# Kernel tuning notes

Hardware: AMD Instinct MI355X
Metric: run time of the kernel (lower is better)

## Reference

```python
import jax, jax.numpy as jnp
import numpy as np

D = 64       # feature_dim
C = 64       # number of classes
NS = 1024    # support samples (16 shots per class)
NQ = 32768   # query samples
REG = 0.3    # reg_param
KAPPA0 = 1.0 / 600.0  # gamma_m from _num_images=600


def _l2norm(x):
    # torch F.normalize(p=2, dim=1) with eps=1e-12
    return x / jnp.maximum(jnp.linalg.norm(x, axis=1, keepdims=True), 1e-12)


def setup_inputs() -> dict:
    key = jax.random.key(0)
    k1, k2 = jax.random.split(key)
    return {
        "X_support": jax.random.normal(k1, (NS, D), dtype=jnp.float32),
        "y_support": jnp.arange(NS, dtype=jnp.int32) % C,  # every class populated
        "X_query": jax.random.normal(k2, (NQ, D), dtype=jnp.float32),
        "m": jnp.zeros((D,), dtype=jnp.float32),            # zeros * gamma_m
        "S": jnp.eye(D, dtype=jnp.float32),                  # eye * gamma_S
        "nu": jnp.float32(float(D)),
        "kappa": jnp.float32(KAPPA0),
    }


def reference(X_support, y_support, X_query, m, S, nu, kappa):
    # ---- fit ----
    Xs = _l2norm(X_support)                                   # [NS, D]
    onehot = jax.nn.one_hot(y_support, C, dtype=Xs.dtype)     # [NS, C]
    Nj = onehot.sum(axis=0)                                   # [C] per-class counts
    means = (onehot.T @ Xs) / Nj[:, None]                     # [C, D] class means
    N0 = Nj[0]                                                # original uses class-0 count
    # head_mu_eq is vector + scalar broadcast, exactly as the torch code
    head = kappa / (kappa + N0) * m + N0 / (kappa + N0)       # [D]
    mu = head[None, :] * means                                # [C, D] elementwise product
    L = S * jnp.tril(jnp.ones((D, D), dtype=Xs.dtype))        # triu(ones).t() mask
    middle = L @ L.T                                          # [D, D]
    Ssum = jnp.einsum('nj,nd,ne->jde', onehot, Xs, Xs)        # sum of outer products per class
    left = 1.0 / (nu + Nj + D + 2)                            # [C]
    mmT = kappa * jnp.outer(m, m)                             # [D, D]
    mu_outer = jnp.einsum('jd,je->jde', mu, mu)               # [C, D, D]
    right = middle[None] + Ssum + mmT[None] - (kappa + Nj)[:, None, None] * mu_outer
    sigma = left[:, None, None] * right                       # [C, D, D]
    A = (1.0 - REG) * jnp.linalg.inv(sigma) + REG * jnp.eye(D, dtype=Xs.dtype)

    # ---- predict: -(x - mu_j)^T A_j (x - mu_j), A_j symmetric ----
    Xq = _l2norm(X_query)                                     # [NQ, D]
    Amu = jnp.einsum('jde,je->jd', A, mu)                     # [C, D]
    cross = Xq @ Amu.T                                        # [NQ, C]
    muAmu = jnp.einsum('jd,jd->j', mu, Amu)                   # [C]
    XA = jnp.einsum('nd,jde->nje', Xq, A)                     # [NQ, C, D]
    quad = jnp.einsum('nje,ne->nj', XA, Xq)                   # [NQ, C]
    return -(quad - 2.0 * cross + muAmu[None, :])             # [NQ, C]
```

## Files before the change

### kernel.cpp

```cpp
#include <hip/hip_runtime.h>
#include <stdint.h>

#define NSUP 1024
#define NQRY 32768
#define DIM  64
#define NCLS 64

typedef float  f32x4  __attribute__((ext_vector_type(4)));
typedef short  s16x8  __attribute__((ext_vector_type(8)));
typedef __bf16 bf16x8 __attribute__((ext_vector_type(8)));

static __device__ __forceinline__ unsigned short f2bf(float f) {
  unsigned u = __float_as_uint(f);
  u += 0x7FFFu + ((u >> 16) & 1u);
  return (unsigned short)(u >> 16);
}

__global__ __launch_bounds__(256) void prep_and_mid(
    const float* __restrict__ Xq, const float* __restrict__ mg,
    const float* __restrict__ Sg, const float* __restrict__ kapg,
    unsigned short* __restrict__ Ybf, float* __restrict__ Mid2) {
  __shared__ float Sls[64 * 65];
  __shared__ float mls[64];
  int tid = threadIdx.x;

  if (blockIdx.x < 2048) {
    int lane = tid & 63;
    int wave = tid >> 6;
    int row  = blockIdx.x * 16 + wave * 4 + (lane >> 4);
    int cb   = (lane & 15) * 4;
    float4 v = *(const float4*)(Xq + (size_t)row * 64 + cb);
    float ss = v.x * v.x + v.y * v.y + v.z * v.z + v.w * v.w;
    ss += __shfl_xor(ss, 1);
    ss += __shfl_xor(ss, 2);
    ss += __shfl_xor(ss, 4);
    ss += __shfl_xor(ss, 8);
    float inv = 1.0f / fmaxf(sqrtf(ss), 1e-12f);
    unsigned short a = f2bf(v.x * inv), b = f2bf(v.y * inv);
    unsigned short c = f2bf(v.z * inv), d = f2bf(v.w * inv);
    uint2 o;
    o.x = (unsigned)a | ((unsigned)b << 16);
    o.y = (unsigned)c | ((unsigned)d << 16);
    *(uint2*)(Ybf + (size_t)row * 64 + cb) = o;
    return;
  }

  for (int i = tid; i < 4096; i += 256) Sls[(i >> 6) * 65 + (i & 63)] = Sg[i];
  if (tid < 64) mls[tid] = mg[tid];
  __syncthreads();
  float kap = kapg[0];
  int r_ = tid & 63, cblk = tid >> 6, c0 = cblk * 16;
#pragma unroll 1
  for (int i = 0; i < 16; ++i) {
    int cc = c0 + i;
    int kmax = min(r_, cc);
    float mid = 0.f;
    for (int k = 0; k <= kmax; ++k) mid += Sls[r_ * 65 + k] * Sls[cc * 65 + k];
    Mid2[r_ * 64 + cc] = mid + kap * mls[r_] * mls[cc];
  }
}

__global__ __launch_bounds__(256) void fit_classes(
    const float* __restrict__ Xs, const int* __restrict__ ys,
    const float* __restrict__ mg, const float* __restrict__ Mid2,
    const float* __restrict__ nug, const float* __restrict__ kapg,
    unsigned short* __restrict__ LtG, float* __restrict__ Bg) {
  __shared__ float xsch[16][68];
  __shared__ float muls[64];
  __shared__ float fcol[2][64];
  __shared__ float prow[2][64];
  __shared__ float Lls[64 * 65];
  __shared__ int   lst[64];
  __shared__ int   cnts[2];

  int tid = threadIdx.x;
  int j   = blockIdx.x;
  int rr = tid >> 2, cq = tid & 3, cc0 = cq * 16;

  if (tid < 64) {
    int lane = tid;
    int cnt = 0, n0 = 0;
    for (int b = 0; b < NSUP; b += 64) {
      int yv = ys[b + lane];
      unsigned long long mj = __ballot(yv == j);
      unsigned long long m0 = __ballot(yv == 0);
      if (lane == 0) {
        n0 += (int)__popcll(m0);
        while (mj && cnt < 64) { int bit = __builtin_ctzll(mj); lst[cnt++] = b + bit; mj &= mj - 1; }
      }
    }
    if (lane == 0) { cnts[0] = cnt; cnts[1] = n0; }
  }
  __syncthreads();
  int cnt = cnts[0], n0 = cnts[1];

  float acc[16];
  {
    const float* mrow = Mid2 + rr * 64 + cc0;
    float4 m0 = *(const float4*)(mrow + 0);
    float4 m1 = *(const float4*)(mrow + 4);
    float4 m2 = *(const float4*)(mrow + 8);
    float4 m3 = *(const float4*)(mrow + 12);
    acc[0]=m0.x; acc[1]=m0.y; acc[2]=m0.z; acc[3]=m0.w;
    acc[4]=m1.x; acc[5]=m1.y; acc[6]=m1.z; acc[7]=m1.w;
    acc[8]=m2.x; acc[9]=m2.y; acc[10]=m2.z; acc[11]=m2.w;
    acc[12]=m3.x; acc[13]=m3.y; acc[14]=m3.z; acc[15]=m3.w;
  }

  float sumx = 0.f;
  for (int s0 = 0; s0 < cnt; s0 += 16) {
    int nch = min(16, cnt - s0);
    int s = tid >> 4, f = tid & 15;
    if (s < nch) {
      int n = lst[s0 + s];
      float4 v = *(const float4*)(Xs + (size_t)n * 64 + f * 4);
      float ss = v.x * v.x + v.y * v.y + v.z * v.z + v.w * v.w;
      ss += __shfl_xor(ss, 1); ss += __shfl_xor(ss, 2);
      ss += __shfl_xor(ss, 4); ss += __shfl_xor(ss, 8);
      float inv = 1.0f / fmaxf(sqrtf(ss), 1e-12f);
      xsch[s][f * 4 + 0] = v.x * inv;
      xsch[s][f * 4 + 1] = v.y * inv;
      xsch[s][f * 4 + 2] = v.z * inv;
      xsch[s][f * 4 + 3] = v.w * inv;
    }
    __syncthreads();
    for (int s2 = 0; s2 < nch; ++s2) {
      float ar = xsch[s2][rr];
      sumx += ar;
#pragma unroll
      for (int i = 0; i < 16; ++i) acc[i] += ar * xsch[s2][cc0 + i];
    }
    __syncthreads();
  }

  float kap = kapg[0], nuv = nug[0];
  float Njf = (float)cnt, N0f = (float)n0;
  float mean_r = sumx / Njf;
  float head_r = kap / (kap + N0f) * mg[rr] + N0f / (kap + N0f);
  float mu_r = head_r * mean_r;
  if (cq == 0) muls[rr] = mu_r;
  __syncthreads();

  float a[16];
  {
    float left = 1.0f / (nuv + Njf + (float)DIM + 2.0f);
    float kn = kap + Njf;
#pragma unroll
    for (int i = 0; i < 16; ++i)
      a[i] = left * (acc[i] - kn * mu_r * muls[cc0 + i]);
  }

  {
    float fsel = 0.f;
#pragma unroll
    for (int i = 0; i < 16; ++i) fsel = (cc0 + i == 0) ? a[i] : fsel;
    if (cq == 0) fcol[0][rr] = fsel;
    if (rr == 0) {
#pragma unroll
      for (int i = 0; i < 16; ++i) prow[0][cc0 + i] = a[i];
    }
  }
  __syncthreads();

  for (int p = 0; p < 64; ++p) {
    int pb = p & 1;
    float d  = 1.0f / fcol[pb][p];
    float fr = fcol[pb][rr];
#pragma unroll
    for (int i = 0; i < 16; ++i) {
      int c = cc0 + i;
      float q  = prow[pb][c] * d;
      float ar = a[i];
      float res;
      if (rr == p) res = (c == p) ? d : q;
      else         res = (c == p) ? (-fr * d) : fmaf(-fr, q, ar);
      a[i] = res;
    }
    if (p < 63) {
      float fsel = 0.f;
#pragma unroll
      for (int i = 0; i < 16; ++i) fsel = (cc0 + i == p + 1) ? a[i] : fsel;
      if (cq == ((p + 1) >> 4)) fcol[pb ^ 1][rr] = fsel;
      if (rr == p + 1) {
#pragma unroll
        for (int i = 0; i < 16; ++i) prow[pb ^ 1][cc0 + i] = a[i];
      }
    }
    __syncthreads();
  }

#pragma unroll
  for (int i = 0; i < 16; ++i)
    a[i] = 0.7f * a[i] + ((cc0 + i == rr) ? 0.3f : 0.f);
  {
    float fsel = 0.f;
#pragma unroll
    for (int i = 0; i < 16; ++i) fsel = (cc0 + i == 0) ? a[i] : fsel;
    if (cq == 0) fcol[0][rr] = fsel;
  }
  __syncthreads();

  for (int k = 0; k < 64; ++k) {
    int pb = k & 1;
    float akk = fcol[pb][k];
    float rs  = 1.0f / sqrtf(akk);
    float vr  = fcol[pb][rr] * rs;
#pragma unroll
    for (int i = 0; i < 16; ++i) {
      int c = cc0 + i;
      if (c == k)              a[i] = (rr >= k) ? vr : 0.f;
      else if (rr > k && c > k) a[i] -= vr * (fcol[pb][c] * rs);
    }
    if (k < 63) {
      float fsel = 0.f;
#pragma unroll
      for (int i = 0; i < 16; ++i) fsel = (cc0 + i == k + 1) ? a[i] : fsel;
      if (cq == ((k + 1) >> 4)) fcol[pb ^ 1][rr] = fsel;
    }
    __syncthreads();
  }

#pragma unroll
  for (int i = 0; i < 16; ++i) {
    int c = cc0 + i;
    Lls[rr * 65 + c] = (c <= rr) ? a[i] : 0.f;
  }
  __syncthreads();
  {
    unsigned short tmp[16];
#pragma unroll
    for (int i = 0; i < 16; ++i) tmp[i] = f2bf(Lls[(cc0 + i) * 65 + rr]);
    uint4 w0, w1;
    w0.x = (unsigned)tmp[0]  | ((unsigned)tmp[1]  << 16);
    w0.y = (unsigned)tmp[2]  | ((unsigned)tmp[3]  << 16);
    w0.z = (unsigned)tmp[4]  | ((unsigned)tmp[5]  << 16);
    w0.w = (unsigned)tmp[6]  | ((unsigned)tmp[7]  << 16);
    w1.x = (unsigned)tmp[8]  | ((unsigned)tmp[9]  << 16);
    w1.y = (unsigned)tmp[10] | ((unsigned)tmp[11] << 16);
    w1.z = (unsigned)tmp[12] | ((unsigned)tmp[13] << 16);
    w1.w = (unsigned)tmp[14] | ((unsigned)tmp[15] << 16);
    *(uint4*)(LtG + j * 4096 + rr * 64 + cc0)     = w0;
    *(uint4*)(LtG + j * 4096 + rr * 64 + cc0 + 8) = w1;
  }
  {
    float s = 0.f;
#pragma unroll
    for (int i = 0; i < 16; ++i) s += Lls[(cc0 + i) * 65 + rr] * muls[cc0 + i];
    s += __shfl_xor(s, 1);
    s += __shfl_xor(s, 2);
    if (cq == 0) Bg[j * 64 + rr] = s;
  }
}

__global__ __launch_bounds__(256) void predict_kernel(
    const unsigned short* __restrict__ Ybf, const unsigned short* __restrict__ Lt,
    const float* __restrict__ Bg, float* __restrict__ out) {
  int tid   = threadIdx.x;
  int lane  = tid & 63;
  int wave  = tid >> 6;
  int qt    = blockIdx.x >> 2;
  int cg    = blockIdx.x & 3;
  int cbase = cg * 16;
  int qbase = qt * 256 + wave * 64;
  int c = lane & 15, h = lane >> 4;

  s16x8 bfr[4][2];
#pragma unroll
  for (int nt = 0; nt < 4; ++nt) {
    const unsigned short* yrow = Ybf + (size_t)(qbase + nt * 16 + c) * 64;
#pragma unroll
    for (int ks = 0; ks < 2; ++ks)
      bfr[nt][ks] = *(const s16x8*)(yrow + ks * 32 + h * 8);
  }

  const unsigned short* ab    = Lt + (size_t)cbase * 4096 + c * 64 + h * 8;
  const float*          bbase = Bg + (size_t)cbase * 64 + h * 4;
  float*                orow  = out + (size_t)(qbase + lane) * 64 + cbase;

#pragma unroll 1
  for (int g = 0; g < 4; ++g) {
    float sc4[4];
#pragma unroll
    for (int u = 0; u < 4; ++u) {
      int jj = g * 4 + u;
      const unsigned short* aj = ab + (size_t)jj * 4096;
      s16x8 af0 = *(const s16x8*)(aj + 0);
      s16x8 af1 = *(const s16x8*)(aj + 1024);
      s16x8 af2 = *(const s16x8*)(aj + 32);
      s16x8 af3 = *(const s16x8*)(aj + 1056);
      s16x8 af4 = *(const s16x8*)(aj + 2080);
      s16x8 af5 = *(const s16x8*)(aj + 3104);
      const float* bb = bbase + (size_t)jj * 64;
      float4 b0 = *(const float4*)(bb);
      float4 b1 = *(const float4*)(bb + 16);
      float4 b2 = *(const float4*)(bb + 32);
      float4 b3 = *(const float4*)(bb + 48);

      float ssel = 0.f;
#pragma unroll
      for (int nt = 0; nt < 4; ++nt) {
        f32x4 a0 = {-b0.x, -b0.y, -b0.z, -b0.w};
        f32x4 a1 = {-b1.x, -b1.y, -b1.z, -b1.w};
        f32x4 a2 = {-b2.x, -b2.y, -b2.z, -b2.w};
        f32x4 a3 = {-b3.x, -b3.y, -b3.z, -b3.w};
        a0 = __builtin_amdgcn_mfma_f32_16x16x32_bf16(
            __builtin_bit_cast(bf16x8, af0), __builtin_bit_cast(bf16x8, bfr[nt][0]), a0, 0, 0, 0);
        a1 = __builtin_amdgcn_mfma_f32_16x16x32_bf16(
            __builtin_bit_cast(bf16x8, af1), __builtin_bit_cast(bf16x8, bfr[nt][0]), a1, 0, 0, 0);
        a0 = __builtin_amdgcn_mfma_f32_16x16x32_bf16(
            __builtin_bit_cast(bf16x8, af2), __builtin_bit_cast(bf16x8, bfr[nt][1]), a0, 0, 0, 0);
        a1 = __builtin_amdgcn_mfma_f32_16x16x32_bf16(
            __builtin_bit_cast(bf16x8, af3), __builtin_bit_cast(bf16x8, bfr[nt][1]), a1, 0, 0, 0);
        a2 = __builtin_amdgcn_mfma_f32_16x16x32_bf16(
            __builtin_bit_cast(bf16x8, af4), __builtin_bit_cast(bf16x8, bfr[nt][1]), a2, 0, 0, 0);
        a3 = __builtin_amdgcn_mfma_f32_16x16x32_bf16(
            __builtin_bit_cast(bf16x8, af5), __builtin_bit_cast(bf16x8, bfr[nt][1]), a3, 0, 0, 0);
        float s = a0[0] * a0[0] + a0[1] * a0[1] + a0[2] * a0[2] + a0[3] * a0[3];
        s += a1[0] * a1[0] + a1[1] * a1[1] + a1[2] * a1[2] + a1[3] * a1[3];
        s += a2[0] * a2[0] + a2[1] * a2[1] + a2[2] * a2[2] + a2[3] * a2[3];
        s += a3[0] * a3[0] + a3[1] * a3[1] + a3[2] * a3[2] + a3[3] * a3[3];
        s += __shfl_xor(s, 16);
        s += __shfl_xor(s, 32);
        if (nt == h) ssel = s;
      }
      sc4[u] = -ssel;
    }
    f32x4 v = { sc4[0], sc4[1], sc4[2], sc4[3] };
    *(f32x4*)(orow + g * 4) = v;
  }
}

extern "C" void kernel_launch(void* const* d_in, const int* in_sizes, int n_in,
                              void* d_out, int out_size, void* d_ws, size_t ws_size,
                              hipStream_t stream) {
  const float* Xs   = (const float*)d_in[0];
  const int*   ys   = (const int*)d_in[1];
  const float* Xq   = (const float*)d_in[2];
  const float* mg   = (const float*)d_in[3];
  const float* Sg   = (const float*)d_in[4];
  const float* nug  = (const float*)d_in[5];
  const float* kapg = (const float*)d_in[6];
  float* out = (float*)d_out;

  unsigned short* Ybf = (unsigned short*)d_ws;
  unsigned short* LtG = Ybf + (size_t)NQRY * 64;
  float* Bg   = (float*)(LtG + (size_t)NCLS * 4096);
  float* Mid2 = Bg + NCLS * 64;

  prep_and_mid<<<dim3(2049), dim3(256), 0, stream>>>(Xq, mg, Sg, kapg, Ybf, Mid2);
  fit_classes<<<dim3(NCLS), dim3(256), 0, stream>>>(Xs, ys, mg, Mid2, nug, kapg,
                                                    LtG, Bg);
  predict_kernel<<<dim3(512), dim3(256), 0, stream>>>(Ybf, LtG, Bg, out);
}
```

Measured before the change: 306.4 us.

## Rewrite per-class fit as single-wave register kernel using readlane broadcasts

The per-class fit kernel moves from 256 threads with shared-memory pivot exchange and a barrier per elimination step to a single 64-lane wave. Each lane holds a full matrix row in registers and gets pivot values through readlane, which removes all barriers in the Gauss-Jordan inversion and the Cholesky loops. Reciprocal and rsqrt use hardware approximations refined by one Newton step. The predict kernel stages its scores in LDS and writes them after the MFMA loop, so the MFMA chain no longer waits on stores. The trade-offs are heavy register pressure from 64-element per-lane arrays, only 64 threads per class in the fit, and slightly different rounding.

```diff
diff --git a/kernel.cpp b/kernel.cpp
--- a/kernel.cpp
+++ b/kernel.cpp
@@ -14,6 +14,17 @@
   unsigned u = __float_as_uint(f);
   u += 0x7FFFu + ((u >> 16) & 1u);
   return (unsigned short)(u >> 16);
+}
+static __device__ __forceinline__ float rl(float v, int l) {
+  return __uint_as_float(__builtin_amdgcn_readlane(__float_as_uint(v), l));
+}
+static __device__ __forceinline__ float rcp_nr(float x) {
+  float r = __builtin_amdgcn_rcpf(x);
+  return r * fmaf(-x, r, 2.0f);
+}
+static __device__ __forceinline__ float rsq_nr(float x) {
+  float r = __builtin_amdgcn_rsqf(x);
+  return r * fmaf(-0.5f * x * r, r, 1.5f);
 }
 
 __global__ __launch_bounds__(256) void prep_and_mid(
@@ -35,7 +46,7 @@
     ss += __shfl_xor(ss, 2);
     ss += __shfl_xor(ss, 4);
     ss += __shfl_xor(ss, 8);
-    float inv = 1.0f / fmaxf(sqrtf(ss), 1e-12f);
+    float inv = rcp_nr(fmaxf(__builtin_amdgcn_sqrtf(ss), 1e-12f));
     unsigned short a = f2bf(v.x * inv), b = f2bf(v.y * inv);
     unsigned short c = f2bf(v.z * inv), d = f2bf(v.w * inv);
     uint2 o;
@@ -60,201 +71,158 @@
   }
 }
 
-__global__ __launch_bounds__(256) void fit_classes(
+__global__ __launch_bounds__(64) void fit_classes(
     const float* __restrict__ Xs, const int* __restrict__ ys,
     const float* __restrict__ mg, const float* __restrict__ Mid2,
     const float* __restrict__ nug, const float* __restrict__ kapg,
     unsigned short* __restrict__ LtG, float* __restrict__ Bg) {
-  __shared__ float xsch[16][68];
-  __shared__ float muls[64];
-  __shared__ float fcol[2][64];
-  __shared__ float prow[2][64];
-  __shared__ float Lls[64 * 65];
-  __shared__ int   lst[64];
-  __shared__ int   cnts[2];
-
-  int tid = threadIdx.x;
-  int j   = blockIdx.x;
-  int rr = tid >> 2, cq = tid & 3, cc0 = cq * 16;
-
-  if (tid < 64) {
-    int lane = tid;
-    int cnt = 0, n0 = 0;
-    for (int b = 0; b < NSUP; b += 64) {
-      int yv = ys[b + lane];
-      unsigned long long mj = __ballot(yv == j);
-      unsigned long long m0 = __ballot(yv == 0);
-      if (lane == 0) {
-        n0 += (int)__popcll(m0);
-        while (mj && cnt < 64) { int bit = __builtin_ctzll(mj); lst[cnt++] = b + bit; mj &= mj - 1; }
-      }
-    }
-    if (lane == 0) { cnts[0] = cnt; cnts[1] = n0; }
+  __shared__ int   lst[NSUP];
+  __shared__ float Lls[64 * 68];
+
+  int r = threadIdx.x;
+  int j = blockIdx.x;
+
+  int cnt = 0, n0 = 0;
+  for (int b = 0; b < NSUP; b += 64) {
+    int yv = ys[b + r];
+    unsigned long long mj = __ballot(yv == j);
+    unsigned long long m0 = __ballot(yv == 0);
+    n0 += (int)__popcll(m0);
+    if (yv == j) {
+      int rank = cnt + (int)__popcll(mj & ((1ull << r) - 1ull));
+      lst[rank] = b + r;
+    }
+    cnt += (int)__popcll(mj);
   }
   __syncthreads();
-  int cnt = cnts[0], n0 = cnts[1];
-
-  float acc[16];
+
+  float a[64];
   {
-    const float* mrow = Mid2 + rr * 64 + cc0;
-    float4 m0 = *(const float4*)(mrow + 0);
-    float4 m1 = *(const float4*)(mrow + 4);
-    float4 m2 = *(const float4*)(mrow + 8);
-    float4 m3 = *(const float4*)(mrow + 12);
-    acc[0]=m0.x; acc[1]=m0.y; acc[2]=m0.z; acc[3]=m0.w;
-    acc[4]=m1.x; acc[5]=m1.y; acc[6]=m1.z; acc[7]=m1.w;
-    acc[8]=m2.x; acc[9]=m2.y; acc[10]=m2.z; acc[11]=m2.w;
-    acc[12]=m3.x; acc[13]=m3.y; acc[14]=m3.z; acc[15]=m3.w;
+    const float* mrow = Mid2 + r * 64;
+#pragma unroll
+    for (int c4 = 0; c4 < 16; ++c4) {
+      float4 v = *(const float4*)(mrow + c4 * 4);
+      a[c4 * 4 + 0] = v.x; a[c4 * 4 + 1] = v.y;
+      a[c4 * 4 + 2] = v.z; a[c4 * 4 + 3] = v.w;
+    }
   }
 
   float sumx = 0.f;
-  for (int s0 = 0; s0 < cnt; s0 += 16) {
-    int nch = min(16, cnt - s0);
-    int s = tid >> 4, f = tid & 15;
-    if (s < nch) {
-      int n = lst[s0 + s];
-      float4 v = *(const float4*)(Xs + (size_t)n * 64 + f * 4);
-      float ss = v.x * v.x + v.y * v.y + v.z * v.z + v.w * v.w;
-      ss += __shfl_xor(ss, 1); ss += __shfl_xor(ss, 2);
-      ss += __shfl_xor(ss, 4); ss += __shfl_xor(ss, 8);
-      float inv = 1.0f / fmaxf(sqrtf(ss), 1e-12f);
-      xsch[s][f * 4 + 0] = v.x * inv;
-      xsch[s][f * 4 + 1] = v.y * inv;
-      xsch[s][f * 4 + 2] = v.z * inv;
-      xsch[s][f * 4 + 3] = v.w * inv;
-    }
-    __syncthreads();
-    for (int s2 = 0; s2 < nch; ++s2) {
-      float ar = xsch[s2][rr];
-      sumx += ar;
-#pragma unroll
-      for (int i = 0; i < 16; ++i) acc[i] += ar * xsch[s2][cc0 + i];
-    }
-    __syncthreads();
+  for (int s = 0; s < cnt; ++s) {
+    int n = lst[s];
+    float v = Xs[(size_t)n * 64 + r];
+    float ss = v * v;
+    ss += __shfl_xor(ss, 1);  ss += __shfl_xor(ss, 2);
+    ss += __shfl_xor(ss, 4);  ss += __shfl_xor(ss, 8);
+    ss += __shfl_xor(ss, 16); ss += __shfl_xor(ss, 32);
+    float inv = rcp_nr(fmaxf(__builtin_amdgcn_sqrtf(ss), 1e-12f));
+    float xn = v * inv;
+    sumx += xn;
+#pragma unroll
+    for (int c = 0; c < 64; ++c) a[c] = fmaf(xn, rl(xn, c), a[c]);
   }
 
   float kap = kapg[0], nuv = nug[0];
   float Njf = (float)cnt, N0f = (float)n0;
-  float mean_r = sumx / Njf;
-  float head_r = kap / (kap + N0f) * mg[rr] + N0f / (kap + N0f);
-  float mu_r = head_r * mean_r;
-  if (cq == 0) muls[rr] = mu_r;
+  float rkn0 = rcp_nr(kap + N0f);
+  float head = kap * rkn0 * mg[r] + N0f * rkn0;
+  float mu = head * (sumx * rcp_nr(Njf));
+
+  {
+    float left = rcp_nr(nuv + Njf + (float)DIM + 2.0f);
+    float t = (kap + Njf) * mu;
+#pragma unroll
+    for (int c = 0; c < 64; ++c)
+      a[c] = left * fmaf(-t, rl(mu, c), a[c]);
+  }
+
+  float fr = a[0];
+  for (int p = 0; p < 64; ++p) {
+    float dval = rl(fr, p);
+    float dinv = rcp_nr(dval);
+    bool isp = (r == p);
+    float frd = fr * dinv;
+    float colp_v = isp ? dinv : -frd;
+    float fnext = 0.f;
+#pragma unroll
+    for (int c = 0; c < 64; ++c) {
+      float pc = rl(a[c], p);
+      float q  = pc * dinv;
+      float nv;
+      if (c == p) {
+        nv = colp_v;
+      } else {
+        float tmp = fmaf(-fr, q, a[c]);
+        nv = isp ? q : tmp;
+      }
+      a[c] = nv;
+      if (c == p + 1) fnext = nv;
+    }
+    fr = fnext;
+  }
+
+#pragma unroll
+  for (int c = 0; c < 64; ++c) {
+    float dd = (c == r) ? 0.3f : 0.f;
+    a[c] = fmaf(0.7f, a[c], dd);
+  }
+
+  float fk = a[0];
+  for (int k = 0; k < 64; ++k) {
+    float akk = rl(fk, k);
+    float rs  = rsq_nr(akk);
+    float lrk = (r >= k) ? fk * rs : 0.f;
+    float fnext = 0.f;
+#pragma unroll
+    for (int c = 0; c < 64; ++c) {
+      float nv;
+      if (c == k) nv = lrk;
+      else        nv = fmaf(-lrk, rl(lrk, c), a[c]);
+      a[c] = nv;
+      if (c == k + 1) fnext = nv;
+    }
+    fk = fnext;
+  }
+
+#pragma unroll
+  for (int c = 0; c < 64; ++c)
+    Lls[r * 68 + c] = (c <= r) ? a[c] : 0.f;
   __syncthreads();
 
-  float a[16];
-  {
-    float left = 1.0f / (nuv + Njf + (float)DIM + 2.0f);
-    float kn = kap + Njf;
-#pragma unroll
-    for (int i = 0; i < 16; ++i)
-      a[i] = left * (acc[i] - kn * mu_r * muls[cc0 + i]);
-  }
-
-  {
-    float fsel = 0.f;
-#pragma unroll
-    for (int i = 0; i < 16; ++i) fsel = (cc0 + i == 0) ? a[i] : fsel;
-    if (cq == 0) fcol[0][rr] = fsel;
-    if (rr == 0) {
-#pragma unroll
-      for (int i = 0; i < 16; ++i) prow[0][cc0 + i] = a[i];
-    }
-  }
-  __syncthreads();
-
-  for (int p = 0; p < 64; ++p) {
-    int pb = p & 1;
-    float d  = 1.0f / fcol[pb][p];
-    float fr = fcol[pb][rr];
-#pragma unroll
-    for (int i = 0; i < 16; ++i) {
-      int c = cc0 + i;
-      float q  = prow[pb][c] * d;
-      float ar = a[i];
-      float res;
-      if (rr == p) res = (c == p) ? d : q;
-      else         res = (c == p) ? (-fr * d) : fmaf(-fr, q, ar);
-      a[i] = res;
-    }
-    if (p < 63) {
-      float fsel = 0.f;
-#pragma unroll
-      for (int i = 0; i < 16; ++i) fsel = (cc0 + i == p + 1) ? a[i] : fsel;
-      if (cq == ((p + 1) >> 4)) fcol[pb ^ 1][rr] = fsel;
-      if (rr == p + 1) {
-#pragma unroll
-        for (int i = 0; i < 16; ++i) prow[pb ^ 1][cc0 + i] = a[i];
-      }
-    }
-    __syncthreads();
-  }
-
-#pragma unroll
-  for (int i = 0; i < 16; ++i)
-    a[i] = 0.7f * a[i] + ((cc0 + i == rr) ? 0.3f : 0.f);
-  {
-    float fsel = 0.f;
-#pragma unroll
-    for (int i = 0; i < 16; ++i) fsel = (cc0 + i == 0) ? a[i] : fsel;
-    if (cq == 0) fcol[0][rr] = fsel;
-  }
-  __syncthreads();
-
-  for (int k = 0; k < 64; ++k) {
-    int pb = k & 1;
-    float akk = fcol[pb][k];
-    float rs  = 1.0f / sqrtf(akk);
-    float vr  = fcol[pb][rr] * rs;
-#pragma unroll
-    for (int i = 0; i < 16; ++i) {
-      int c = cc0 + i;
-      if (c == k)              a[i] = (rr >= k) ? vr : 0.f;
-      else if (rr > k && c > k) a[i] -= vr * (fcol[pb][c] * rs);
-    }
-    if (k < 63) {
-      float fsel = 0.f;
-#pragma unroll
-      for (int i = 0; i < 16; ++i) fsel = (cc0 + i == k + 1) ? a[i] : fsel;
-      if (cq == ((k + 1) >> 4)) fcol[pb ^ 1][rr] = fsel;
-    }
-    __syncthreads();
-  }
-
-#pragma unroll
-  for (int i = 0; i < 16; ++i) {
-    int c = cc0 + i;
-    Lls[rr * 65 + c] = (c <= rr) ? a[i] : 0.f;
-  }
-  __syncthreads();
-  {
-    unsigned short tmp[16];
-#pragma unroll
-    for (int i = 0; i < 16; ++i) tmp[i] = f2bf(Lls[(cc0 + i) * 65 + rr]);
-    uint4 w0, w1;
-    w0.x = (unsigned)tmp[0]  | ((unsigned)tmp[1]  << 16);
-    w0.y = (unsigned)tmp[2]  | ((unsigned)tmp[3]  << 16);
-    w0.z = (unsigned)tmp[4]  | ((unsigned)tmp[5]  << 16);
-    w0.w = (unsigned)tmp[6]  | ((unsigned)tmp[7]  << 16);
-    w1.x = (unsigned)tmp[8]  | ((unsigned)tmp[9]  << 16);
-    w1.y = (unsigned)tmp[10] | ((unsigned)tmp[11] << 16);
-    w1.z = (unsigned)tmp[12] | ((unsigned)tmp[13] << 16);
-    w1.w = (unsigned)tmp[14] | ((unsigned)tmp[15] << 16);
-    *(uint4*)(LtG + j * 4096 + rr * 64 + cc0)     = w0;
-    *(uint4*)(LtG + j * 4096 + rr * 64 + cc0 + 8) = w1;
-  }
-  {
-    float s = 0.f;
-#pragma unroll
-    for (int i = 0; i < 16; ++i) s += Lls[(cc0 + i) * 65 + rr] * muls[cc0 + i];
-    s += __shfl_xor(s, 1);
-    s += __shfl_xor(s, 2);
-    if (cq == 0) Bg[j * 64 + rr] = s;
-  }
+  unsigned short* lrow = LtG + (size_t)j * 4096 + r * 64;
+  float bias = 0.f;
+#pragma unroll
+  for (int u = 0; u < 8; ++u) {
+    float v0 = Lls[(u * 8 + 0) * 68 + r];
+    float v1 = Lls[(u * 8 + 1) * 68 + r];
+    float v2 = Lls[(u * 8 + 2) * 68 + r];
+    float v3 = Lls[(u * 8 + 3) * 68 + r];
+    float v4 = Lls[(u * 8 + 4) * 68 + r];
+    float v5 = Lls[(u * 8 + 5) * 68 + r];
+    float v6 = Lls[(u * 8 + 6) * 68 + r];
+    float v7 = Lls[(u * 8 + 7) * 68 + r];
+    bias = fmaf(v0, rl(mu, u * 8 + 0), bias);
+    bias = fmaf(v1, rl(mu, u * 8 + 1), bias);
+    bias = fmaf(v2, rl(mu, u * 8 + 2), bias);
+    bias = fmaf(v3, rl(mu, u * 8 + 3), bias);
+    bias = fmaf(v4, rl(mu, u * 8 + 4), bias);
+    bias = fmaf(v5, rl(mu, u * 8 + 5), bias);
+    bias = fmaf(v6, rl(mu, u * 8 + 6), bias);
+    bias = fmaf(v7, rl(mu, u * 8 + 7), bias);
+    uint4 w;
+    w.x = (unsigned)f2bf(v0) | ((unsigned)f2bf(v1) << 16);
+    w.y = (unsigned)f2bf(v2) | ((unsigned)f2bf(v3) << 16);
+    w.z = (unsigned)f2bf(v4) | ((unsigned)f2bf(v5) << 16);
+    w.w = (unsigned)f2bf(v6) | ((unsigned)f2bf(v7) << 16);
+    *(uint4*)(lrow + u * 8) = w;
+  }
+  Bg[j * 64 + r] = bias;
 }
 
 __global__ __launch_bounds__(256) void predict_kernel(
     const unsigned short* __restrict__ Ybf, const unsigned short* __restrict__ Lt,
     const float* __restrict__ Bg, float* __restrict__ out) {
+  __shared__ float scl[256 * 17];
   int tid   = threadIdx.x;
   int lane  = tid & 63;
   int wave  = tid >> 6;
@@ -275,57 +243,58 @@
 
   const unsigned short* ab    = Lt + (size_t)cbase * 4096 + c * 64 + h * 8;
   const float*          bbase = Bg + (size_t)cbase * 64 + h * 4;
-  float*                orow  = out + (size_t)(qbase + lane) * 64 + cbase;
+  float*                sbase = &scl[tid * 17];
 
 #pragma unroll 1
+  for (int jj = 0; jj < 16; ++jj) {
+    const unsigned short* aj = ab + (size_t)jj * 4096;
+    s16x8 af0 = *(const s16x8*)(aj + 0);
+    s16x8 af1 = *(const s16x8*)(aj + 1024);
+    s16x8 af2 = *(const s16x8*)(aj + 32);
+    s16x8 af3 = *(const s16x8*)(aj + 1056);
+    s16x8 af4 = *(const s16x8*)(aj + 2080);
+    s16x8 af5 = *(const s16x8*)(aj + 3104);
+    const float* bb = bbase + (size_t)jj * 64;
+    float4 b0 = *(const float4*)(bb);
+    float4 b1 = *(const float4*)(bb + 16);
+    float4 b2 = *(const float4*)(bb + 32);
+    float4 b3 = *(const float4*)(bb + 48);
+    f32x4 nb0 = {-b0.x, -b0.y, -b0.z, -b0.w};
+    f32x4 nb1 = {-b1.x, -b1.y, -b1.z, -b1.w};
+    f32x4 nb2 = {-b2.x, -b2.y, -b2.z, -b2.w};
+    f32x4 nb3 = {-b3.x, -b3.y, -b3.z, -b3.w};
+
+    float ssel = 0.f;
+#pragma unroll
+    for (int nt = 0; nt < 4; ++nt) {
+      f32x4 a0 = __builtin_amdgcn_mfma_f32_16x16x32_bf16(
+          __builtin_bit_cast(bf16x8, af0), __builtin_bit_cast(bf16x8, bfr[nt][0]), nb0, 0, 0, 0);
+      a0 = __builtin_amdgcn_mfma_f32_16x16x32_bf16(
+          __builtin_bit_cast(bf16x8, af2), __builtin_bit_cast(bf16x8, bfr[nt][1]), a0, 0, 0, 0);
+      f32x4 a1 = __builtin_amdgcn_mfma_f32_16x16x32_bf16(
+          __builtin_bit_cast(bf16x8, af1), __builtin_bit_cast(bf16x8, bfr[nt][0]), nb1, 0, 0, 0);
+      a1 = __builtin_amdgcn_mfma_f32_16x16x32_bf16(
+          __builtin_bit_cast(bf16x8, af3), __builtin_bit_cast(bf16x8, bfr[nt][1]), a1, 0, 0, 0);
+      f32x4 a2 = __builtin_amdgcn_mfma_f32_16x16x32_bf16(
+          __builtin_bit_cast(bf16x8, af4), __builtin_bit_cast(bf16x8, bfr[nt][1]), nb2, 0, 0, 0);
+      f32x4 a3 = __builtin_amdgcn_mfma_f32_16x16x32_bf16(
+          __builtin_bit_cast(bf16x8, af5), __builtin_bit_cast(bf16x8, bfr[nt][1]), nb3, 0, 0, 0);
+      float s = a0[0] * a0[0] + a0[1] * a0[1] + a0[2] * a0[2] + a0[3] * a0[3];
+      s += a1[0] * a1[0] + a1[1] * a1[1] + a1[2] * a1[2] + a1[3] * a1[3];
+      s += a2[0] * a2[0] + a2[1] * a2[1] + a2[2] * a2[2] + a2[3] * a2[3];
+      s += a3[0] * a3[0] + a3[1] * a3[1] + a3[2] * a3[2] + a3[3] * a3[3];
+      s += __shfl_xor(s, 16);
+      s += __shfl_xor(s, 32);
+      if (nt == h) ssel = s;
+    }
+    sbase[jj] = -ssel;
+  }
+
+  float* orow = out + (size_t)(qbase + lane) * 64 + cbase;
+#pragma unroll
   for (int g = 0; g < 4; ++g) {
-    float sc4[4];
-#pragma unroll
-    for (int u = 0; u < 4; ++u) {
-      int jj = g * 4 + u;
-      const unsigned short* aj = ab + (size_t)jj * 4096;
-      s16x8 af0 = *(const s16x8*)(aj + 0);
-      s16x8 af1 = *(const s16x8*)(aj + 1024);
-      s16x8 af2 = *(const s16x8*)(aj + 32);
-      s16x8 af3 = *(const s16x8*)(aj + 1056);
-      s16x8 af4 = *(const s16x8*)(aj + 2080);
-      s16x8 af5 = *(const s16x8*)(aj + 3104);
-      const float* bb = bbase + (size_t)jj * 64;
-      float4 b0 = *(const float4*)(bb);
-      float4 b1 = *(const float4*)(bb + 16);
-      float4 b2 = *(const float4*)(bb + 32);
-      float4 b3 = *(const float4*)(bb + 48);
-
-      float ssel = 0.f;
-#pragma unroll
-      for (int nt = 0; nt < 4; ++nt) {
-        f32x4 a0 = {-b0.x, -b0.y, -b0.z, -b0.w};
-        f32x4 a1 = {-b1.x, -b1.y, -b1.z, -b1.w};
-        f32x4 a2 = {-b2.x, -b2.y, -b2.z, -b2.w};
-        f32x4 a3 = {-b3.x, -b3.y, -b3.z, -b3.w};
-        a0 = __builtin_amdgcn_mfma_f32_16x16x32_bf16(
-            __builtin_bit_cast(bf16x8, af0), __builtin_bit_cast(bf16x8, bfr[nt][0]), a0, 0, 0, 0);
-        a1 = __builtin_amdgcn_mfma_f32_16x16x32_bf16(
-            __builtin_bit_cast(bf16x8, af1), __builtin_bit_cast(bf16x8, bfr[nt][0]), a1, 0, 0, 0);
-        a0 = __builtin_amdgcn_mfma_f32_16x16x32_bf16(
-            __builtin_bit_cast(bf16x8, af2), __builtin_bit_cast(bf16x8, bfr[nt][1]), a0, 0, 0, 0);
-        a1 = __builtin_amdgcn_mfma_f32_16x16x32_bf16(
-            __builtin_bit_cast(bf16x8, af3), __builtin_bit_cast(bf16x8, bfr[nt][1]), a1, 0, 0, 0);
-        a2 = __builtin_amdgcn_mfma_f32_16x16x32_bf16(
-            __builtin_bit_cast(bf16x8, af4), __builtin_bit_cast(bf16x8, bfr[nt][1]), a2, 0, 0, 0);
-        a3 = __builtin_amdgcn_mfma_f32_16x16x32_bf16(
-            __builtin_bit_cast(bf16x8, af5), __builtin_bit_cast(bf16x8, bfr[nt][1]), a3, 0, 0, 0);
-        float s = a0[0] * a0[0] + a0[1] * a0[1] + a0[2] * a0[2] + a0[3] * a0[3];
-        s += a1[0] * a1[0] + a1[1] * a1[1] + a1[2] * a1[2] + a1[3] * a1[3];
-        s += a2[0] * a2[0] + a2[1] * a2[1] + a2[2] * a2[2] + a2[3] * a2[3];
-        s += a3[0] * a3[0] + a3[1] * a3[1] + a3[2] * a3[2] + a3[3] * a3[3];
-        s += __shfl_xor(s, 16);
-        s += __shfl_xor(s, 32);
-        if (nt == h) ssel = s;
-      }
-      sc4[u] = -ssel;
-    }
-    f32x4 v = { sc4[0], sc4[1], sc4[2], sc4[3] };
+    f32x4 v = { sbase[g * 4 + 0], sbase[g * 4 + 1],
+                sbase[g * 4 + 2], sbase[g * 4 + 3] };
     *(f32x4*)(orow + g * 4) = v;
   }
 }
@@ -348,7 +317,7 @@
   float* Mid2 = Bg + NCLS * 64;
 
   prep_and_mid<<<dim3(2049), dim3(256), 0, stream>>>(Xq, mg, Sg, kapg, Ybf, Mid2);
-  fit_classes<<<dim3(NCLS), dim3(256), 0, stream>>>(Xs, ys, mg, Mid2, nug, kapg,
-                                                    LtG, Bg);
+  fit_classes<<<dim3(NCLS), dim3(64), 0, stream>>>(Xs, ys, mg, Mid2, nug, kapg,
+                                                   LtG, Bg);
   predict_kernel<<<dim3(512), dim3(256), 0, stream>>>(Ybf, LtG, Bg, out);
 }
```

Measured after the change: 318.6 us. 1.04x slower.
